# Optimization experiments

Hardware: AMD Instinct MI355X
Metric: run time of the kernel (lower is better)

The kernel has to match this reference:

```python
import jax, jax.numpy as jnp
import numpy as np

WH, WW = 12, 12          # window height/width
N = WH * WW              # tokens per window (144)
HEADS = 16
DIM = 1024
C = DIM // 2             # attention channel dim (512)
HEAD_DIM = C // HEADS    # 32


def _rel_pos_index(wh, ww):
    ch, cw = np.arange(wh), np.arange(ww)
    coords = np.stack(np.meshgrid(ch, cw, indexing='ij')).reshape(2, -1)  # [2, N]
    rel = (coords[:, :, None] - coords[:, None, :]).transpose(1, 2, 0)    # [N, N, 2]
    rel = rel.copy()
    rel[:, :, 0] += wh - 1
    rel[:, :, 1] += ww - 1
    rel[:, :, 0] *= 2 * ww - 1
    return rel.sum(-1)  # [N, N] int


def _layernorm(x, g, b, eps=1e-5):
    mu = jnp.mean(x, axis=-1, keepdims=True)
    var = jnp.mean(jnp.square(x - mu), axis=-1, keepdims=True)
    return (x - mu) * jax.lax.rsqrt(var + eps) * g + b


def setup_inputs():
    key = jax.random.key(0)
    ks = jax.random.split(key, 10)
    std = 0.02
    inp = {
        'x': jax.random.normal(ks[0], (256, N, DIM), jnp.float32),
        'template': jax.random.normal(ks[1], (64, N, DIM), jnp.float32),
        'mask0': jnp.zeros((16, N, N), jnp.float32),
        'mask1': jnp.zeros((4, N, N), jnp.float32),
        's_H': 48, 's_W': 48, 't_H': 24, 't_W': 24,
        'rpb_table': jax.random.normal(ks[2], ((2 * WH - 1) * (2 * WW - 1), HEADS), jnp.float32) * std,
        'w_ps': jax.random.normal(ks[3], (DIM, C), jnp.float32) * std,
        'b_ps': jnp.zeros((C,), jnp.float32),
        'g_ps': jnp.ones((C,), jnp.float32),
        'be_ps': jnp.zeros((C,), jnp.float32),
        'w_pt': jax.random.normal(ks[4], (DIM, C), jnp.float32) * std,
        'b_pt': jnp.zeros((C,), jnp.float32),
        'g_pt': jnp.ones((C,), jnp.float32),
        'be_pt': jnp.zeros((C,), jnp.float32),
        'w_qkv': jax.random.normal(ks[5], (C, 3 * C), jnp.float32) * std,
        'b_qkv': jnp.zeros((3 * C,), jnp.float32),
        'w_tr': jax.random.normal(ks[6], (C, DIM), jnp.float32) * std,
        'b_tr': jnp.zeros((DIM,), jnp.float32),
        'w_sr': jax.random.normal(ks[7], (C, DIM), jnp.float32) * std,
        'b_sr': jnp.zeros((DIM,), jnp.float32),
    }
    return inp


def reference(x, template, mask0, mask1, s_H, s_W, t_H, t_W,
              rpb_table, w_ps, b_ps, g_ps, be_ps, w_pt, b_pt, g_pt, be_pt,
              w_qkv, b_qkv, w_tr, b_tr, w_sr, b_sr):
    scale = HEAD_DIM ** (-0.5)
    search_attn = _layernorm(x @ w_ps + b_ps, g_ps, be_ps)          # [Sw, N, C]
    template_attn = _layernorm(template @ w_pt + b_pt, g_pt, be_pt)  # [Tw, N, C]
    Sw, Tw = search_attn.shape[0], template_attn.shape[0]
    xa = jnp.concatenate([template_attn, search_attn], axis=0)      # [B_, N, C]
    B_, n, c = xa.shape

    qkv = (xa @ w_qkv + b_qkv).reshape(B_, n, 3, HEADS, HEAD_DIM)
    q = qkv[:, :, 0].transpose(0, 2, 1, 3) * scale  # [B_, H, N, Dh]
    k = qkv[:, :, 1].transpose(0, 2, 1, 3)
    v = qkv[:, :, 2].transpose(0, 2, 1, 3)

    idx = _rel_pos_index(WH, WW)  # numpy constant [N, N]
    bias = rpb_table[idx.reshape(-1)].reshape(n, n, HEADS).transpose(2, 0, 1)  # [H, N, N]

    attn = jnp.einsum('bhnd,bhmd->bhnm', q, k) + bias[None]  # [B_, H, N, N]

    attn_t, attn_s = attn[:Tw], attn[Tw:]
    nWs = mask0.shape[0]
    attn_s = (attn_s.reshape(Sw // nWs, nWs, HEADS, n, n) + mask0[None, :, None]).reshape(Sw, HEADS, n, n)
    nWt = mask1.shape[0]
    attn_t = (attn_t.reshape(Tw // nWt, nWt, HEADS, n, n) + mask1[None, :, None]).reshape(Tw, HEADS, n, n)
    attn = jax.nn.softmax(jnp.concatenate([attn_t, attn_s], axis=0), axis=-1)

    out = jnp.einsum('bhnm,bhmd->bhnd', attn, v).transpose(0, 2, 1, 3).reshape(B_, n, c)
    template_out = out[:Tw] @ w_tr + b_tr  # [Tw, N, DIM]
    search_out = out[Tw:] @ w_sr + b_sr    # [Sw, N, DIM]
    return (template_out, search_out)
```

## Files before the change

kernel.cpp:

```cpp
#include <hip/hip_runtime.h>


using s16x8 = __attribute__((ext_vector_type(8))) short;
using f32x4 = __attribute__((ext_vector_type(4))) float;
typedef __attribute__((ext_vector_type(2))) unsigned u32x2;

#define NTOK 144
#define NHEADS 16
#define CDIM 512
#define TROWS 9216
#define SROWS 36864
#define TOTROWS 46080
#define NWIN 320
#define NCLS 20

__device__ __forceinline__ unsigned short f2bf(float f) {
  unsigned u = __float_as_uint(f);
  u += 0x7fffu + ((u >> 16) & 1u);
  return (unsigned short)(u >> 16);
}
__device__ __forceinline__ float bf2f(unsigned short u) {
  return __uint_as_float(((unsigned)u) << 16);
}
__device__ __forceinline__ s16x8 mk8(unsigned a, unsigned b, unsigned c, unsigned d) {
  union { unsigned u[4]; s16x8 v; } x;
  x.u[0] = a; x.u[1] = b; x.u[2] = c; x.u[3] = d;
  return x.v;
}

__device__ __forceinline__ void gld16(const void* g, void* l) {
  __builtin_amdgcn_global_load_lds(
      (const __attribute__((address_space(1))) unsigned int*)g,
      (__attribute__((address_space(3))) unsigned int*)l, 16, 0, 0);
}


__global__ void transpose_cast(const float* __restrict__ w,
                               unsigned short* __restrict__ wT, int Kd, int Nd,
                               int nScale, float s) {
  int i = blockIdx.x * 256 + threadIdx.x;
  if (i >= Kd * Nd) return;
  int n = i / Kd, k = i % Kd;
  float v = w[(size_t)k * Nd + n];
  if (n < nScale) v *= s;
  wT[i] = f2bf(v);
}

__global__ void scale_bias(const float* __restrict__ in, float* __restrict__ out) {
  int i = blockIdx.x * 256 + threadIdx.x;
  if (i >= 1536) return;
  out[i] = in[i] * (i < 512 ? 0.17677669529663687f : 1.0f);
}

__global__ __launch_bounds__(256) void cast_bf16(const float* __restrict__ in,
                                                 unsigned short* __restrict__ out, int n8) {
  int i = blockIdx.x * 256 + threadIdx.x;
  if (i >= n8) return;
  const float4* p = (const float4*)in + (size_t)i * 2;
  float4 f0 = p[0], f1 = p[1];
  s16x8 o;
  o[0] = (short)f2bf(f0.x); o[1] = (short)f2bf(f0.y);
  o[2] = (short)f2bf(f0.z); o[3] = (short)f2bf(f0.w);
  o[4] = (short)f2bf(f1.x); o[5] = (short)f2bf(f1.y);
  o[6] = (short)f2bf(f1.z); o[7] = (short)f2bf(f1.w);
  *(s16x8*)&out[(size_t)i * 8] = o;
}

__global__ void build_cmb(const float* __restrict__ rpb, const float* __restrict__ m0,
                          const float* __restrict__ m1, unsigned short* __restrict__ cmb) {
  int i = blockIdx.x * 256 + threadIdx.x;
  if (i >= NCLS * NHEADS * NTOK * NTOK) return;
  int cls = i / (NHEADS * NTOK * NTOK);
  int rem = i % (NHEADS * NTOK * NTOK);
  int h = rem / (NTOK * NTOK);
  int ij = rem % (NTOK * NTOK);
  int qi = ij / NTOK, kj = ij % NTOK;
  int dh = qi / 12 - kj / 12 + 11;
  int dw = qi % 12 - kj % 12 + 11;
  float bias = rpb[(dh * 23 + dw) * NHEADS + h];
  float mv = (cls < 4) ? m1[(size_t)cls * NTOK * NTOK + ij]
                       : m0[(size_t)(cls - 4) * NTOK * NTOK + ij];
  cmb[i] = f2bf(bias + mv);
}

template<int EPI>
__global__ __launch_bounds__(512, 2) void gemm256(
    const unsigned short* __restrict__ Ab,
    const unsigned short* __restrict__ BTt, const unsigned short* __restrict__ BTs,
    const float* __restrict__ biast, const float* __restrict__ biass,
    void* __restrict__ Cout, int M, int N, int K)
{
  extern __shared__ short smem[];
  const int t = threadIdx.x;
  const int lane = t & 63, wv = t >> 6, lg = lane >> 4, lc = lane & 15;
  const int wr = wv >> 2, wc = wv & 3;

  const int id = blockIdx.x + gridDim.x * blockIdx.y;
  const int chunk = (gridDim.x * gridDim.y) >> 3;
  const int lid = (id & 7) * chunk + (id >> 3);
  const int bn = (lid % gridDim.x) * 256, bm = (lid / gridDim.x) * 256;

  const bool isT = bm < TROWS;
  const unsigned short* BT = isT ? BTt : BTs;
  const float* bias = isT ? biast : biass;

  const int srow = 32 * wv + (lane >> 3);
  const int scol = ((lane & 7) ^ ((lane >> 3) & 7)) * 8;
  const unsigned short* aSrc = Ab + (size_t)(bm + srow) * K + scol;
  const unsigned short* bSrc = BT + (size_t)(bn + srow) * K + scol;
  const size_t rowK8 = (size_t)8 * K;

  f32x4 acc[8][4] = {};

  auto STAGE = [&](int b, int kt) {
    short* Asb = smem + b * 16384;
    short* Bsb = smem + 32768 + b * 16384;
#pragma unroll
    for (int i = 0; i < 4; i++) {
      gld16(aSrc + kt + i * rowK8, Asb + (wv * 4 + i) * 512);
      gld16(bSrc + kt + i * rowK8, Bsb + (wv * 4 + i) * 512);
    }
  };
  auto COMPUTE = [&](int b) {
    const short* Asb = smem + b * 16384;
    const short* Bsb = smem + 32768 + b * 16384;
#pragma unroll
    for (int kk = 0; kk < 2; kk++) {
      const int csw = 8 * ((4 * kk + lg) ^ (lc & 7));
      s16x8 bf[4];
#pragma unroll
      for (int c = 0; c < 4; c++)
        bf[c] = *(const s16x8*)&Bsb[(wc * 64 + c * 16 + lc) * 64 + csw];
#pragma unroll
      for (int r = 0; r < 8; r++) {
        s16x8 af = *(const s16x8*)&Asb[(wr * 128 + r * 16 + lc) * 64 + csw];
#pragma unroll
        for (int c = 0; c < 4; c++)
          acc[r][c] = __builtin_amdgcn_mfma_f32_16x16x32_bf16(af, bf[c], acc[r][c], 0, 0, 0);
      }
    }
  };

  STAGE(0, 0);
  int cur = 0;
  for (int kt = 64; kt < K; kt += 64) {
    STAGE(cur ^ 1, kt);
    asm volatile("s_waitcnt vmcnt(8)" ::: "memory");
    __builtin_amdgcn_s_barrier();
    __builtin_amdgcn_sched_barrier(0);
    COMPUTE(cur);
    __builtin_amdgcn_s_barrier();
    cur ^= 1;
  }
  asm volatile("s_waitcnt vmcnt(0)" ::: "memory");
  __builtin_amdgcn_s_barrier();
  __builtin_amdgcn_sched_barrier(0);
  COMPUTE(cur);

#pragma unroll
  for (int r = 0; r < 8; r++) {
    const int rbase = bm + wr * 128 + r * 16 + lg * 4;
#pragma unroll
    for (int c = 0; c < 4; c++) {
      const int cg = bn + wc * 64 + c * 16 + lc;
#pragma unroll
      for (int rr = 0; rr < 4; rr++) {
        float val = acc[r][c][rr] + bias[cg];
        if (EPI == 2) ((float*)Cout)[(size_t)(rbase + rr) * N + cg] = val;
        else ((unsigned short*)Cout)[(size_t)(rbase + rr) * N + cg] = f2bf(val);
      }
    }
  }
}

__global__ __launch_bounds__(256) void ln_kernel(
    unsigned short* __restrict__ xa,
    const float* __restrict__ g_pt, const float* __restrict__ be_pt,
    const float* __restrict__ g_ps, const float* __restrict__ be_ps)
{
  const int row = blockIdx.x * 4 + (threadIdx.x >> 6);
  const int lane = threadIdx.x & 63;
  const bool isT = row < TROWS;
  const float* gg = isT ? g_pt : g_ps;
  const float* be = isT ? be_pt : be_ps;
  unsigned short* p = xa + (size_t)row * CDIM;
  const int c0 = lane * 8;

  s16x8 v8 = *(const s16x8*)&p[c0];
  float f[8];
  float s = 0.f, s2 = 0.f;
#pragma unroll
  for (int i = 0; i < 8; i++) {
    float xv = bf2f((unsigned short)v8[i]);
    f[i] = xv; s += xv; s2 += xv * xv;
  }
#pragma unroll
  for (int d = 1; d < 64; d <<= 1) { s += __shfl_xor(s, d); s2 += __shfl_xor(s2, d); }
  float mu = s * (1.f / CDIM);
  float var = s2 * (1.f / CDIM) - mu * mu;
  float rs = rsqrtf(var + 1e-5f);

  float4 g0 = *(const float4*)&gg[c0], g1 = *(const float4*)&gg[c0 + 4];
  float4 e0 = *(const float4*)&be[c0], e1 = *(const float4*)&be[c0 + 4];
  float gv[8] = {g0.x, g0.y, g0.z, g0.w, g1.x, g1.y, g1.z, g1.w};
  float ev[8] = {e0.x, e0.y, e0.z, e0.w, e1.x, e1.y, e1.z, e1.w};
  s16x8 o;
#pragma unroll
  for (int i = 0; i < 8; i++)
    o[i] = (short)f2bf((f[i] - mu) * rs * gv[i] + ev[i]);
  *(s16x8*)&p[c0] = o;
}

__global__ __launch_bounds__(576) void attn_kernel(
    const unsigned short* __restrict__ qkv, const unsigned short* __restrict__ cmb,
    unsigned short* __restrict__ outp)
{
  __shared__ short VT[32 * 168];
  const int nb = NWIN * NHEADS;
  const int lid = (blockIdx.x & 7) * (nb >> 3) + (blockIdx.x >> 3);
  const int w = lid >> 4, h = lid & 15;
  const int t = threadIdx.x;
  const unsigned short* qb = qkv + (size_t)w * NTOK * 1536;
  const int hq = h * 32;

  {
    const int n = t >> 2, d0 = (t & 3) * 8;
    s16x8 vv = *(const s16x8*)&qb[(size_t)n * 1536 + 1024 + hq + d0];
#pragma unroll
    for (int i = 0; i < 8; i++) VT[(d0 + i) * 168 + n] = vv[i];
  }
  if (t < 512) VT[(t >> 4) * 168 + 144 + (t & 15)] = 0;

  const int lane = t & 63, wv = t >> 6, lg = lane >> 4, lc = lane & 15;
  const int q = wv * 16 + lc;
  const f32x4 zero = {0.f, 0.f, 0.f, 0.f};

  const s16x8 qf = *(const s16x8*)&qb[(size_t)q * 1536 + hq + lg * 8];

  const int cls = (w < 64) ? (w & 3) : 4 + ((w - 64) & 15);
  const unsigned short* cm =
      cmb + ((size_t)cls * NHEADS + h) * (NTOK * NTOK) + (size_t)q * NTOK;
  uint2 cmr[9];
#pragma unroll
  for (int nt = 0; nt < 9; nt++)
    cmr[nt] = *(const uint2*)&cm[nt * 16 + lg * 4];

  f32x4 accS[9];
  __builtin_amdgcn_s_setprio(1);
#pragma unroll
  for (int nt = 0; nt < 9; nt++) {
    s16x8 kf = *(const s16x8*)&qb[(size_t)(nt * 16 + lc) * 1536 + 512 + hq + lg * 8];
    accS[nt] = __builtin_amdgcn_mfma_f32_16x16x32_bf16(kf, qf, zero, 0, 0, 0);
  }
  __builtin_amdgcn_s_setprio(0);

  float mx = -1e30f;
#pragma unroll
  for (int nt = 0; nt < 9; nt++) {
    accS[nt][0] += bf2f((unsigned short)(cmr[nt].x & 0xffff));
    accS[nt][1] += bf2f((unsigned short)(cmr[nt].x >> 16));
    accS[nt][2] += bf2f((unsigned short)(cmr[nt].y & 0xffff));
    accS[nt][3] += bf2f((unsigned short)(cmr[nt].y >> 16));
#pragma unroll
    for (int r = 0; r < 4; r++) mx = fmaxf(mx, accS[nt][r]);
  }
  mx = fmaxf(mx, __shfl_xor(mx, 16));
  mx = fmaxf(mx, __shfl_xor(mx, 32));

  float sum = 0.f;
#pragma unroll
  for (int nt = 0; nt < 9; nt++)
#pragma unroll
    for (int r = 0; r < 4; r++) {
      float e = __expf(accS[nt][r] - mx);
      accS[nt][r] = e;
      sum += e;
    }
  sum += __shfl_xor(sum, 16);
  sum += __shfl_xor(sum, 32);
  const float inv = 1.f / sum;

  unsigned pk0[9], pk1[9];
#pragma unroll
  for (int nt = 0; nt < 9; nt++) {
    pk0[nt] = (unsigned)f2bf(accS[nt][0]) | ((unsigned)f2bf(accS[nt][1]) << 16);
    pk1[nt] = (unsigned)f2bf(accS[nt][2]) | ((unsigned)f2bf(accS[nt][3]) << 16);
  }

  __syncthreads();

  __builtin_amdgcn_s_setprio(1);
#pragma unroll
  for (int dt = 0; dt < 2; dt++) {
    const short* vbase = &VT[(dt * 16 + lc) * 168];
    f32x4 accO = zero;
#pragma unroll
    for (int kk = 0; kk < 4; kk++) {
      u32x2 A0 = *(const u32x2*)&vbase[32 * kk + lg * 4];
      u32x2 A1 = *(const u32x2*)&vbase[32 * kk + 16 + lg * 4];
      s16x8 a = mk8(A0[0], A0[1], A1[0], A1[1]);
      s16x8 b = mk8(pk0[2 * kk], pk1[2 * kk], pk0[2 * kk + 1], pk1[2 * kk + 1]);
      accO = __builtin_amdgcn_mfma_f32_16x16x32_bf16(a, b, accO, 0, 0, 0);
    }
    {
      u32x2 A0 = *(const u32x2*)&vbase[128 + lg * 4];
      s16x8 a = mk8(A0[0], A0[1], 0u, 0u);
      s16x8 b = mk8(pk0[8], pk1[8], 0u, 0u);
      accO = __builtin_amdgcn_mfma_f32_16x16x32_bf16(a, b, accO, 0, 0, 0);
    }
    unsigned o0 = (unsigned)f2bf(accO[0] * inv) | ((unsigned)f2bf(accO[1] * inv) << 16);
    unsigned o1 = (unsigned)f2bf(accO[2] * inv) | ((unsigned)f2bf(accO[3] * inv) << 16);
    uint2 st; st.x = o0; st.y = o1;
    *(uint2*)&outp[(size_t)(w * NTOK + q) * CDIM + hq + dt * 16 + lg * 4] = st;
  }
  __builtin_amdgcn_s_setprio(0);
}

extern "C" void kernel_launch(void* const* d_in, const int* in_sizes, int n_in,
                              void* d_out, int out_size, void* d_ws, size_t ws_size,
                              hipStream_t stream)
{
  const float* x     = (const float*)d_in[0];
  const float* tpl   = (const float*)d_in[1];
  const float* mask0 = (const float*)d_in[2];
  const float* mask1 = (const float*)d_in[3];
  const float* rpb   = (const float*)d_in[8];
  const float* w_ps  = (const float*)d_in[9];
  const float* b_ps  = (const float*)d_in[10];
  const float* g_ps  = (const float*)d_in[11];
  const float* be_ps = (const float*)d_in[12];
  const float* w_pt  = (const float*)d_in[13];
  const float* b_pt  = (const float*)d_in[14];
  const float* g_pt  = (const float*)d_in[15];
  const float* be_pt = (const float*)d_in[16];
  const float* w_qkv = (const float*)d_in[17];
  const float* b_qkv = (const float*)d_in[18];
  const float* w_tr  = (const float*)d_in[19];
  const float* b_tr  = (const float*)d_in[20];
  const float* w_sr  = (const float*)d_in[21];
  const float* b_sr  = (const float*)d_in[22];

  char* ws = (char*)d_ws;
  unsigned short* wpsT  = (unsigned short*)(ws + 0x0000000);
  unsigned short* wptT  = (unsigned short*)(ws + 0x0100000);
  unsigned short* wqkvT = (unsigned short*)(ws + 0x0200000);
  unsigned short* wtrT  = (unsigned short*)(ws + 0x0380000);
  unsigned short* wsrT  = (unsigned short*)(ws + 0x0480000);
  unsigned short* cmb   = (unsigned short*)(ws + 0x0580000);
  float* bqS            = (float*)(ws + 0x12F0000);
  unsigned short* xa    = (unsigned short*)(ws + 0x1300000);
  unsigned short* Sa    = (unsigned short*)(ws + 0x4000000);
  unsigned short* qkvF  = (unsigned short*)(ws + 0x4000000);
  float* outb           = (float*)d_out;

  hipFuncSetAttribute((const void*)gemm256<0>,
                      hipFuncAttributeMaxDynamicSharedMemorySize, 131072);
  hipFuncSetAttribute((const void*)gemm256<2>,
                      hipFuncAttributeMaxDynamicSharedMemorySize, 131072);

  transpose_cast<<<2048, 256, 0, stream>>>(w_ps, wpsT, 1024, 512, 0, 1.f);
  transpose_cast<<<2048, 256, 0, stream>>>(w_pt, wptT, 1024, 512, 0, 1.f);
  transpose_cast<<<3072, 256, 0, stream>>>(w_qkv, wqkvT, 512, 1536,
                                           512, 0.17677669529663687f);
  transpose_cast<<<2048, 256, 0, stream>>>(w_tr, wtrT, 512, 1024, 0, 1.f);
  transpose_cast<<<2048, 256, 0, stream>>>(w_sr, wsrT, 512, 1024, 0, 1.f);
  scale_bias<<<6, 256, 0, stream>>>(b_qkv, bqS);
  build_cmb<<<(NCLS * NHEADS * NTOK * NTOK + 255) / 256, 256, 0, stream>>>(rpb, mask0, mask1, cmb);

  cast_bf16<<<(TROWS * 1024 / 8 + 255) / 256, 256, 0, stream>>>(tpl, Sa, TROWS * 1024 / 8);
  cast_bf16<<<(SROWS * 1024 / 8 + 255) / 256, 256, 0, stream>>>(
      x, Sa + (size_t)TROWS * 1024, SROWS * 1024 / 8);

  gemm256<0><<<dim3(2, 180), 512, 131072, stream>>>(Sa, wptT, wpsT, b_pt, b_ps,
                                                    xa, TOTROWS, CDIM, 1024);
  ln_kernel<<<TOTROWS / 4, 256, 0, stream>>>(xa, g_pt, be_pt, g_ps, be_ps);

  gemm256<0><<<dim3(6, 180), 512, 131072, stream>>>(xa, wqkvT, wqkvT, bqS, bqS,
                                                    qkvF, TOTROWS, 1536, CDIM);
  attn_kernel<<<NWIN * NHEADS, 576, 0, stream>>>(qkvF, cmb, xa);

  gemm256<2><<<dim3(4, 180), 512, 131072, stream>>>(xa, wtrT, wsrT, b_tr, b_sr,
                                                    outb, TOTROWS, 1024, CDIM);
}
```

Measured before the change: 453.1 us.

## Interleave quarter-tile global-to-LDS staging with quadrant MFMA phases in GEMM

Measured after the change: 465.3 us. 2.7% more time.

```diff
diff --git a/kernel.cpp b/kernel.cpp
--- a/kernel.cpp
+++ b/kernel.cpp
@@ -104,58 +104,88 @@
   const unsigned short* BT = isT ? BTt : BTs;
   const float* bias = isT ? biast : biass;
 
-  const int srow = 32 * wv + (lane >> 3);
-  const int scol = ((lane & 7) ^ ((lane >> 3) & 7)) * 8;
-  const unsigned short* aSrc = Ab + (size_t)(bm + srow) * K + scol;
-  const unsigned short* bSrc = BT + (size_t)(bn + srow) * K + scol;
-  const size_t rowK8 = (size_t)8 * K;
+  const int sr8 = lane >> 3;
+  const int scg = ((lane & 7) ^ ((lane >> 3) & 7)) * 8;
 
   f32x4 acc[8][4] = {};
 
-  auto STAGE = [&](int b, int kt) {
-    short* Asb = smem + b * 16384;
-    short* Bsb = smem + 32768 + b * 16384;
-#pragma unroll
-    for (int i = 0; i < 4; i++) {
-      gld16(aSrc + kt + i * rowK8, Asb + (wv * 4 + i) * 512);
-      gld16(bSrc + kt + i * rowK8, Bsb + (wv * 4 + i) * 512);
-    }
+  auto STAGE = [&](int ph, int sl, int kt) {
+    const int h = ph & 1;
+    const int rbase = h * 128 + wv * 16;
+    const unsigned short* src;
+    short* dst;
+    if (ph < 2) {
+      src = Ab + (size_t)(bm + rbase + sr8) * K + kt + scg;
+      dst = smem + sl * 16384 + rbase * 64;
+    } else {
+      src = BT + (size_t)(bn + rbase + sr8) * K + kt + scg;
+      dst = smem + 32768 + sl * 16384 + rbase * 64;
+    }
+    gld16(src, dst);
+    gld16(src + (size_t)8 * K, dst + 8 * 64);
   };
-  auto COMPUTE = [&](int b) {
-    const short* Asb = smem + b * 16384;
-    const short* Bsb = smem + 32768 + b * 16384;
-#pragma unroll
-    for (int kk = 0; kk < 2; kk++) {
-      const int csw = 8 * ((4 * kk + lg) ^ (lc & 7));
-      s16x8 bf[4];
-#pragma unroll
-      for (int c = 0; c < 4; c++)
-        bf[c] = *(const s16x8*)&Bsb[(wc * 64 + c * 16 + lc) * 64 + csw];
-#pragma unroll
-      for (int r = 0; r < 8; r++) {
-        s16x8 af = *(const s16x8*)&Asb[(wr * 128 + r * 16 + lc) * 64 + csw];
-#pragma unroll
-        for (int c = 0; c < 4; c++)
-          acc[r][c] = __builtin_amdgcn_mfma_f32_16x16x32_bf16(af, bf[c], acc[r][c], 0, 0, 0);
+
+  STAGE(0, 0, 0); STAGE(1, 0, 0); STAGE(2, 0, 0); STAGE(3, 0, 0);
+
+  const int T = K >> 6;
+  int s = 0;
+  for (int kt = 0; kt < K; kt += 64) {
+    const int ktn = (kt + 64 < K) ? kt + 64 : kt;
+    const short* Asl = smem + s * 16384;
+    const short* Bsl = smem + 32768 + s * 16384;
+#pragma unroll
+    for (int q = 0; q < 4; ++q) {
+      const int a = q >> 1, b = q & 1;
+      s16x8 af[4][2], bf[2][2];
+      if (q == 0) {
+        STAGE(0, s ^ 1, ktn);
+        asm volatile("s_waitcnt vmcnt(2)" ::: "memory");
+        __builtin_amdgcn_s_barrier();
+        asm volatile("" ::: "memory");
+#pragma unroll
+        for (int kk = 0; kk < 2; kk++) {
+          const int csw = 8 * ((4 * kk + lg) ^ (lc & 7));
+#pragma unroll
+          for (int j = 0; j < 4; j++)
+            af[j][kk] = *(const s16x8*)&Asl[(wr * 128 + (4 * a + j) * 16 + lc) * 64 + csw];
+#pragma unroll
+          for (int cc = 0; cc < 2; cc++)
+            bf[cc][kk] = *(const s16x8*)&Bsl[(wc * 64 + (2 * b + cc) * 16 + lc) * 64 + csw];
+        }
+      } else {
+#pragma unroll
+        for (int kk = 0; kk < 2; kk++) {
+          const int csw = 8 * ((4 * kk + lg) ^ (lc & 7));
+#pragma unroll
+          for (int j = 0; j < 4; j++)
+            af[j][kk] = *(const s16x8*)&Asl[(wr * 128 + (4 * a + j) * 16 + lc) * 64 + csw];
+#pragma unroll
+          for (int cc = 0; cc < 2; cc++)
+            bf[cc][kk] = *(const s16x8*)&Bsl[(wc * 64 + (2 * b + cc) * 16 + lc) * 64 + csw];
+        }
+        STAGE(q, s ^ 1, ktn);
+        asm volatile("" ::: "memory");
+        __builtin_amdgcn_s_barrier();
+        asm volatile("" ::: "memory");
       }
-    }
-  };
-
-  STAGE(0, 0);
-  int cur = 0;
-  for (int kt = 64; kt < K; kt += 64) {
-    STAGE(cur ^ 1, kt);
-    asm volatile("s_waitcnt vmcnt(8)" ::: "memory");
-    __builtin_amdgcn_s_barrier();
-    __builtin_amdgcn_sched_barrier(0);
-    COMPUTE(cur);
-    __builtin_amdgcn_s_barrier();
-    cur ^= 1;
+      __builtin_amdgcn_s_setprio(1);
+#pragma unroll
+      for (int j = 0; j < 4; j++)
+#pragma unroll
+        for (int cc = 0; cc < 2; cc++)
+#pragma unroll
+          for (int kk = 0; kk < 2; kk++)
+            acc[4 * a + j][2 * b + cc] = __builtin_amdgcn_mfma_f32_16x16x32_bf16(
+                af[j][kk], bf[cc][kk], acc[4 * a + j][2 * b + cc], 0, 0, 0);
+      __builtin_amdgcn_s_setprio(0);
+      asm volatile("" ::: "memory");
+      __builtin_amdgcn_s_barrier();
+      asm volatile("" ::: "memory");
+    }
+    s ^= 1;
   }
   asm volatile("s_waitcnt vmcnt(0)" ::: "memory");
-  __builtin_amdgcn_s_barrier();
-  __builtin_amdgcn_sched_barrier(0);
-  COMPUTE(cur);
+  (void)T;
 
 #pragma unroll
   for (int r = 0; r < 8; r++) {
```

## Make GEMM kernels persistent with a grid-stride loop over output tiles

Applied to the files above, without the earlier changes.

Result: no change. 455.4 us (+0.5%).

```diff
diff --git a/kernel.cpp b/kernel.cpp
--- a/kernel.cpp
+++ b/kernel.cpp
@@ -84,90 +84,93 @@
 }
 
 template<int EPI>
-__global__ __launch_bounds__(512, 2) void gemm256(
+__global__ __launch_bounds__(512, 1) void gemm256(
     const unsigned short* __restrict__ Ab,
     const unsigned short* __restrict__ BTt, const unsigned short* __restrict__ BTs,
     const float* __restrict__ biast, const float* __restrict__ biass,
-    void* __restrict__ Cout, int M, int N, int K)
+    void* __restrict__ Cout, int gx, int nTiles, int M, int N, int K)
 {
   extern __shared__ short smem[];
   const int t = threadIdx.x;
   const int lane = t & 63, wv = t >> 6, lg = lane >> 4, lc = lane & 15;
   const int wr = wv >> 2, wc = wv & 3;
 
-  const int id = blockIdx.x + gridDim.x * blockIdx.y;
-  const int chunk = (gridDim.x * gridDim.y) >> 3;
-  const int lid = (id & 7) * chunk + (id >> 3);
-  const int bn = (lid % gridDim.x) * 256, bm = (lid / gridDim.x) * 256;
-
-  const bool isT = bm < TROWS;
-  const unsigned short* BT = isT ? BTt : BTs;
-  const float* bias = isT ? biast : biass;
-
-  const int srow = 32 * wv + (lane >> 3);
-  const int scol = ((lane & 7) ^ ((lane >> 3) & 7)) * 8;
-  const unsigned short* aSrc = Ab + (size_t)(bm + srow) * K + scol;
-  const unsigned short* bSrc = BT + (size_t)(bn + srow) * K + scol;
+  const int chunk = nTiles >> 3;
+  const int srowW = 32 * wv + (lane >> 3);
+  const int scg = ((lane & 7) ^ ((lane >> 3) & 7)) * 8;
   const size_t rowK8 = (size_t)8 * K;
 
-  f32x4 acc[8][4] = {};
-
-  auto STAGE = [&](int b, int kt) {
-    short* Asb = smem + b * 16384;
-    short* Bsb = smem + 32768 + b * 16384;
-#pragma unroll
-    for (int i = 0; i < 4; i++) {
-      gld16(aSrc + kt + i * rowK8, Asb + (wv * 4 + i) * 512);
-      gld16(bSrc + kt + i * rowK8, Bsb + (wv * 4 + i) * 512);
-    }
-  };
-  auto COMPUTE = [&](int b) {
-    const short* Asb = smem + b * 16384;
-    const short* Bsb = smem + 32768 + b * 16384;
-#pragma unroll
-    for (int kk = 0; kk < 2; kk++) {
-      const int csw = 8 * ((4 * kk + lg) ^ (lc & 7));
-      s16x8 bf[4];
-#pragma unroll
-      for (int c = 0; c < 4; c++)
-        bf[c] = *(const s16x8*)&Bsb[(wc * 64 + c * 16 + lc) * 64 + csw];
-#pragma unroll
-      for (int r = 0; r < 8; r++) {
-        s16x8 af = *(const s16x8*)&Asb[(wr * 128 + r * 16 + lc) * 64 + csw];
+  for (int tau = blockIdx.x; tau < nTiles; tau += gridDim.x) {
+    const int lid = (tau & 7) * chunk + (tau >> 3);
+    const int bn = (lid % gx) * 256, bm = (lid / gx) * 256;
+
+    const bool isT = bm < TROWS;
+    const unsigned short* BT = isT ? BTt : BTs;
+    const float* bias = isT ? biast : biass;
+
+    const unsigned short* aSrc = Ab + (size_t)(bm + srowW) * K + scg;
+    const unsigned short* bSrc = BT + (size_t)(bn + srowW) * K + scg;
+
+    f32x4 acc[8][4] = {};
+
+    auto STAGE = [&](int b, int kt) {
+      short* Asb = smem + b * 16384;
+      short* Bsb = smem + 32768 + b * 16384;
+#pragma unroll
+      for (int i = 0; i < 4; i++) {
+        gld16(aSrc + kt + i * rowK8, Asb + (wv * 4 + i) * 512);
+        gld16(bSrc + kt + i * rowK8, Bsb + (wv * 4 + i) * 512);
+      }
+    };
+    auto COMPUTE = [&](int b) {
+      const short* Asb = smem + b * 16384;
+      const short* Bsb = smem + 32768 + b * 16384;
+#pragma unroll
+      for (int kk = 0; kk < 2; kk++) {
+        const int csw = 8 * ((4 * kk + lg) ^ (lc & 7));
+        s16x8 bf[4];
 #pragma unroll
         for (int c = 0; c < 4; c++)
-          acc[r][c] = __builtin_amdgcn_mfma_f32_16x16x32_bf16(af, bf[c], acc[r][c], 0, 0, 0);
+          bf[c] = *(const s16x8*)&Bsb[(wc * 64 + c * 16 + lc) * 64 + csw];
+#pragma unroll
+        for (int r = 0; r < 8; r++) {
+          s16x8 af = *(const s16x8*)&Asb[(wr * 128 + r * 16 + lc) * 64 + csw];
+#pragma unroll
+          for (int c = 0; c < 4; c++)
+            acc[r][c] = __builtin_amdgcn_mfma_f32_16x16x32_bf16(af, bf[c], acc[r][c], 0, 0, 0);
+        }
       }
-    }
-  };
-
-  STAGE(0, 0);
-  int cur = 0;
-  for (int kt = 64; kt < K; kt += 64) {
-    STAGE(cur ^ 1, kt);
-    asm volatile("s_waitcnt vmcnt(8)" ::: "memory");
+    };
+
+    __builtin_amdgcn_s_barrier();
+    STAGE(0, 0);
+    int cur = 0;
+    for (int kt = 64; kt < K; kt += 64) {
+      STAGE(cur ^ 1, kt);
+      asm volatile("s_waitcnt vmcnt(8)" ::: "memory");
+      __builtin_amdgcn_s_barrier();
+      __builtin_amdgcn_sched_barrier(0);
+      COMPUTE(cur);
+      __builtin_amdgcn_s_barrier();
+      cur ^= 1;
+    }
+    asm volatile("s_waitcnt vmcnt(0)" ::: "memory");
     __builtin_amdgcn_s_barrier();
     __builtin_amdgcn_sched_barrier(0);
     COMPUTE(cur);
-    __builtin_amdgcn_s_barrier();
-    cur ^= 1;
-  }
-  asm volatile("s_waitcnt vmcnt(0)" ::: "memory");
-  __builtin_amdgcn_s_barrier();
-  __builtin_amdgcn_sched_barrier(0);
-  COMPUTE(cur);
-
-#pragma unroll
-  for (int r = 0; r < 8; r++) {
-    const int rbase = bm + wr * 128 + r * 16 + lg * 4;
-#pragma unroll
-    for (int c = 0; c < 4; c++) {
-      const int cg = bn + wc * 64 + c * 16 + lc;
-#pragma unroll
-      for (int rr = 0; rr < 4; rr++) {
-        float val = acc[r][c][rr] + bias[cg];
-        if (EPI == 2) ((float*)Cout)[(size_t)(rbase + rr) * N + cg] = val;
-        else ((unsigned short*)Cout)[(size_t)(rbase + rr) * N + cg] = f2bf(val);
+
+#pragma unroll
+    for (int r = 0; r < 8; r++) {
+      const int rbase = bm + wr * 128 + r * 16 + lg * 4;
+#pragma unroll
+      for (int c = 0; c < 4; c++) {
+        const int cg = bn + wc * 64 + c * 16 + lc;
+#pragma unroll
+        for (int rr = 0; rr < 4; rr++) {
+          float val = acc[r][c][rr] + bias[cg];
+          if (EPI == 2) ((float*)Cout)[(size_t)(rbase + rr) * N + cg] = val;
+          else ((unsigned short*)Cout)[(size_t)(rbase + rr) * N + cg] = f2bf(val);
+        }
       }
     }
   }
@@ -371,14 +374,14 @@
   cast_bf16<<<(SROWS * 1024 / 8 + 255) / 256, 256, 0, stream>>>(
       x, Sa + (size_t)TROWS * 1024, SROWS * 1024 / 8);
 
-  gemm256<0><<<dim3(2, 180), 512, 131072, stream>>>(Sa, wptT, wpsT, b_pt, b_ps,
-                                                    xa, TOTROWS, CDIM, 1024);
+  gemm256<0><<<256, 512, 131072, stream>>>(Sa, wptT, wpsT, b_pt, b_ps,
+                                           xa, 2, 360, TOTROWS, CDIM, 1024);
   ln_kernel<<<TOTROWS / 4, 256, 0, stream>>>(xa, g_pt, be_pt, g_ps, be_ps);
 
-  gemm256<0><<<dim3(6, 180), 512, 131072, stream>>>(xa, wqkvT, wqkvT, bqS, bqS,
-                                                    qkvF, TOTROWS, 1536, CDIM);
+  gemm256<0><<<256, 512, 131072, stream>>>(xa, wqkvT, wqkvT, bqS, bqS,
+                                           qkvF, 6, 1080, TOTROWS, 1536, CDIM);
   attn_kernel<<<NWIN * NHEADS, 576, 0, stream>>>(qkvF, cmb, xa);
 
-  gemm256<2><<<dim3(4, 180), 512, 131072, stream>>>(xa, wtrT, wsrT, b_tr, b_sr,
-                                                    outb, TOTROWS, 1024, CDIM);
-}
+  gemm256<2><<<256, 512, 131072, stream>>>(xa, wtrT, wsrT, b_tr, b_sr,
+                                           outb, 4, 720, TOTROWS, 1024, CDIM);
+}
```
